# Kernel tuning notes

Hardware: AMD Instinct MI355X
Metric: run time of the kernel (lower is better)

The kernel has to match this reference:

```python
import jax, jax.numpy as jnp
import numpy as np

N, D = 8192, 4096


def setup_inputs() -> dict:
    key = jax.random.key(0)
    k1, k2, k3 = jax.random.split(key, 3)
    x = jax.random.normal(k1, (N, D), jnp.float32)
    W = jax.random.normal(k2, (D, D), jnp.float32) / np.sqrt(D)  # nn.Linear weight [out,in]
    b = jax.random.normal(k3, (D,), jnp.float32) * 0.01
    recency_weight = jnp.full((1,), -0.1, jnp.float32)
    return {"x": x, "W": W, "b": b, "recency_weight": recency_weight}


def reference(x, W, b, recency_weight):
    # linear -> relu projection
    x_proj = jax.nn.relu(x @ W.T + b)  # [N, D]
    # self-similarity
    scores = x_proj @ x_proj.T  # [N, N]
    n = scores.shape[0]
    idx = jnp.arange(n)
    # triu mask with diagonal=0 (use_current_timestep=False): keep strictly lower triangle
    mask = idx[None, :] >= idx[:, None]
    scores = jnp.where(mask, -jnp.inf, scores)
    # recency bias: toeplitz(arange(n)) == |i - j|, zeroed on masked positions
    rec = jnp.abs(idx[:, None] - idx[None, :]).astype(scores.dtype)
    rec = jnp.where(mask, 0.0, rec)
    scores = scores + recency_weight[0] * rec
    # row 0 is fully masked (-inf everywhere); replace with finite values to avoid
    # NaN in softmax -- the row is overwritten with zeros afterwards anyway.
    scores = scores.at[0].set(0.0)
    attn = jax.nn.softmax(scores, axis=1)
    attn = attn.at[0].set(0.0)  # matches scores[0] = zeros in the torch code
    return attn
```

## Files before the change

### kernel.cpp

```cpp
#include <hip/hip_runtime.h>
#include <hip/hip_bf16.h>
#include <stdint.h>

typedef __bf16 bf16_t;
typedef bf16_t bf16x8_t __attribute__((ext_vector_type(8)));
typedef bf16_t bf16x4_t __attribute__((ext_vector_type(4)));
typedef float f32x4_t __attribute__((ext_vector_type(4)));

#define NROWS 8192
#define DDIM  4096
#define BK 32
#define KTILES (DDIM / BK)
#define LSTR 40

__device__ __forceinline__ void gload16(const void* g, void* s) {
  __builtin_amdgcn_global_load_lds(
      (const __attribute__((address_space(1))) void*)g,
      (__attribute__((address_space(3))) void*)s, 16, 0, 0);
}

__global__ __launch_bounds__(256) void k_split(const float* __restrict__ in,
                                               bf16_t* __restrict__ hi,
                                               bf16_t* __restrict__ lo) {
  const long i = ((long)blockIdx.x * 256 + threadIdx.x) * 4;
  const float4 v = *reinterpret_cast<const float4*>(in + i);
  float vv[4] = {v.x, v.y, v.z, v.w};
  bf16x4_t h, l;
#pragma unroll
  for (int c = 0; c < 4; ++c) {
    bf16_t hh = (bf16_t)vv[c];
    h[c] = hh;
    l[c] = (bf16_t)(vv[c] - (float)hh);
  }
  *reinterpret_cast<bf16x4_t*>(hi + i) = h;
  *reinterpret_cast<bf16x4_t*>(lo + i) = l;
}

typedef bf16_t lds_buf_t[4][256][BK];

__device__ __forceinline__ void gemm_core256(
    const bf16_t* __restrict__ pAh, const bf16_t* __restrict__ pAl, long lda,
    const bf16_t* __restrict__ pBh, const bf16_t* __restrict__ pBl, long ldb,
    lds_buf_t* sm, f32x4_t (&acc)[8][4]) {
  const int t = threadIdx.x, lane = t & 63, w = t >> 6;
  const int fr = lane & 15, kg = lane >> 4;
  const int wr = (w >> 2) * 128, wc = (w & 3) * 64;
  const int w32 = w * 32;
  const int sr0 = w32 + (lane >> 2);
  const int sg = (((lane & 3) ^ ((lane >> 3) & 3)) * 8);
  const int kge = (kg ^ ((fr >> 1) & 3)) * 8;

#pragma unroll
  for (int m = 0; m < 8; ++m)
#pragma unroll
    for (int n = 0; n < 4; ++n) acc[m][n] = f32x4_t{0.f, 0.f, 0.f, 0.f};

  const bf16_t* gAh = pAh + (long)sr0 * lda + sg;
  const bf16_t* gAl = pAl + (long)sr0 * lda + sg;
  const bf16_t* gBh = pBh + (long)sr0 * ldb + sg;
  const bf16_t* gBl = pBl + (long)sr0 * ldb + sg;
  const long a16 = 16 * lda, b16 = 16 * ldb;

  auto issue = [&](int buf, int plane, const bf16_t* g, long ld16, int k0) {
    gload16(g + k0, &sm[buf][plane][w32][0]);
    gload16(g + ld16 + k0, &sm[buf][plane][w32 + 16][0]);
  };

  bf16x8_t ah[8], al[8], bh[4], bl[4];
  auto read8 = [&](bf16x8_t(&R)[8], int buf, int plane) {
#pragma unroll
    for (int m = 0; m < 8; ++m)
      R[m] = *reinterpret_cast<const bf16x8_t*>(&sm[buf][plane][wr + m * 16 + fr][kge]);
  };
  auto read4 = [&](bf16x8_t(&R)[4], int buf, int plane) {
#pragma unroll
    for (int n = 0; n < 4; ++n)
      R[n] = *reinterpret_cast<const bf16x8_t*>(&sm[buf][plane][wc + n * 16 + fr][kge]);
  };
  auto mfma32 = [&](bf16x8_t(&A)[8], bf16x8_t(&B)[4]) {
    __builtin_amdgcn_s_setprio(1);
#pragma unroll
    for (int m = 0; m < 8; ++m)
#pragma unroll
      for (int n = 0; n < 4; ++n)
        acc[m][n] = __builtin_amdgcn_mfma_f32_16x16x32_bf16(A[m], B[n], acc[m][n], 0, 0, 0);
    __builtin_amdgcn_s_setprio(0);
  };

  issue(0, 0, gAh, a16, 0);
  issue(0, 2, gBh, b16, 0);
  issue(0, 3, gBl, b16, 0);
  issue(0, 1, gAl, a16, 0);
  asm volatile("s_waitcnt vmcnt(4)" ::: "memory");
  __builtin_amdgcn_s_barrier();

  for (int kt = 0; kt < KTILES - 1; ++kt) {
    const int c = kt & 1;
    const int k0 = (kt + 1) * BK;
    read8(ah, c, 0);
    read4(bh, c, 2);
    issue(c ^ 1, 0, gAh, a16, k0);
    issue(c ^ 1, 2, gBh, b16, k0);
    __builtin_amdgcn_s_barrier();
    mfma32(ah, bh);
    asm volatile("s_waitcnt vmcnt(6)" ::: "memory");
    __builtin_amdgcn_s_barrier();
    read4(bl, c, 3);
    issue(c ^ 1, 3, gBl, b16, k0);
    __builtin_amdgcn_s_barrier();
    mfma32(ah, bl);
    asm volatile("s_waitcnt vmcnt(6)" ::: "memory");
    __builtin_amdgcn_s_barrier();
    read8(al, c, 1);
    issue(c ^ 1, 1, gAl, a16, k0);
    __builtin_amdgcn_s_barrier();
    mfma32(al, bh);
    asm volatile("s_waitcnt vmcnt(4)" ::: "memory");
    __builtin_amdgcn_s_barrier();
  }
  {
    const int c = (KTILES - 1) & 1;
    read8(ah, c, 0);
    read4(bh, c, 2);
    __builtin_amdgcn_s_barrier();
    mfma32(ah, bh);
    asm volatile("s_waitcnt vmcnt(2)" ::: "memory");
    __builtin_amdgcn_s_barrier();
    read4(bl, c, 3);
    __builtin_amdgcn_s_barrier();
    mfma32(ah, bl);
    asm volatile("s_waitcnt vmcnt(0)" ::: "memory");
    __builtin_amdgcn_s_barrier();
    read8(al, c, 1);
    mfma32(al, bh);
  }
}

__global__ __launch_bounds__(512, 2) void k_gemm1_256(
    const bf16_t* __restrict__ xh, const bf16_t* __restrict__ xl,
    const bf16_t* __restrict__ Wh, const bf16_t* __restrict__ Wl,
    const float* __restrict__ bias,
    bf16_t* __restrict__ xph, bf16_t* __restrict__ xpl) {
  extern __shared__ char smraw[];
  lds_buf_t* sm = (lds_buf_t*)smraw;

  int bid = (int)blockIdx.x;
  bid = (bid & 7) * 64 + (bid >> 3);
  const int bx = bid & 15, by = bid >> 4;
  const long brow = (long)by * 256, bcol = (long)bx * 256;

  f32x4_t acc[8][4];
  gemm_core256(xh + brow * DDIM, xl + brow * DDIM, DDIM,
               Wh + bcol * DDIM, Wl + bcol * DDIM, DDIM, sm, acc);

  const int t = threadIdx.x, lane = t & 63, w = t >> 6;
  const int wr = (w >> 2) * 128, wc = (w & 3) * 64;
  const int cr = (lane >> 4) * 4, cc = lane & 15;
#pragma unroll
  for (int n = 0; n < 4; ++n) {
    const long col = bcol + wc + n * 16 + cc;
    const float bb = bias[col];
#pragma unroll
    for (int m = 0; m < 8; ++m) {
      const long row0 = brow + wr + m * 16 + cr;
#pragma unroll
      for (int r = 0; r < 4; ++r) {
        const float v = fmaxf(acc[m][n][r] + bb, 0.f);
        const bf16_t h = (bf16_t)v;
        xph[(row0 + r) * (long)DDIM + col] = h;
        xpl[(row0 + r) * (long)DDIM + col] = (bf16_t)(v - (float)h);
      }
    }
  }
}

__global__ __launch_bounds__(512, 2) void k_gemm2_256(
    const bf16_t* __restrict__ xph, const bf16_t* __restrict__ xpl,
    const float* __restrict__ rwp, float* __restrict__ out) {
  extern __shared__ char smraw[];
  lds_buf_t* sm = (lds_buf_t*)smraw;

  int bid = (int)blockIdx.x;
  bid = (bid & 7) * 66 + (bid >> 3);
  int by = (int)((sqrtf(8.f * (float)bid + 1.f) - 1.f) * 0.5f);
  while ((by + 1) * (by + 2) / 2 <= bid) ++by;
  while (by * (by + 1) / 2 > bid) --by;
  const int bx = bid - by * (by + 1) / 2;

  const long brow = (long)by * 256, bcol = (long)bx * 256;
  f32x4_t acc[8][4];
  gemm_core256(xph + brow * DDIM, xpl + brow * DDIM, DDIM,
               xph + bcol * DDIM, xpl + bcol * DDIM, DDIM, sm, acc);

  const float rw = rwp[0];
  const int t = threadIdx.x, lane = t & 63, w = t >> 6;
  const int wr = (w >> 2) * 128, wc = (w & 3) * 64;
  const int cr = (lane >> 4) * 4, cc = lane & 15;
#pragma unroll
  for (int n = 0; n < 4; ++n) {
    const long gj = bcol + wc + n * 16 + cc;
#pragma unroll
    for (int m = 0; m < 8; ++m) {
      const long gi0 = brow + wr + m * 16 + cr;
#pragma unroll
      for (int r = 0; r < 4; ++r) {
        const long gi = gi0 + r;
        out[gi * (long)NROWS + gj] = acc[m][n][r] + rw * (float)(gi - gj);
      }
    }
  }
}

__device__ __forceinline__ void stage_split(const float* __restrict__ src, long ld,
                                            bf16_t (&hi)[128][LSTR],
                                            bf16_t (&lo)[128][LSTR],
                                            int t) {
#pragma unroll
  for (int i = 0; i < 4; ++i) {
    const int f = i * 256 + t;
    const int row = f >> 3;
    const int kq = (f & 7) << 2;
    const float4 v = *reinterpret_cast<const float4*>(src + (long)row * ld + kq);
    float vv[4] = {v.x, v.y, v.z, v.w};
    bf16x4_t h, l;
#pragma unroll
    for (int c = 0; c < 4; ++c) {
      bf16_t hh = (bf16_t)vv[c];
      h[c] = hh;
      l[c] = (bf16_t)(vv[c] - (float)hh);
    }
    *reinterpret_cast<bf16x4_t*>(&hi[row][kq]) = h;
    *reinterpret_cast<bf16x4_t*>(&lo[row][kq]) = l;
  }
}

__global__ __launch_bounds__(256) void k_gemm1_slow(
    const float* __restrict__ x, const float* __restrict__ W,
    const float* __restrict__ bias,
    bf16_t* __restrict__ xph, bf16_t* __restrict__ xpl) {
  __shared__ alignas(16) bf16_t Ahi[128][LSTR];
  __shared__ alignas(16) bf16_t Alo[128][LSTR];
  __shared__ alignas(16) bf16_t Bhi[128][LSTR];
  __shared__ alignas(16) bf16_t Blo[128][LSTR];

  const long brow = (long)blockIdx.y * 128;
  const long bcol = (long)blockIdx.x * 128;
  const int t = threadIdx.x, lane = t & 63;
  const int wr = ((t >> 6) >> 1) * 64, wc = ((t >> 6) & 1) * 64;
  const int fr = lane & 15, kg = lane >> 4;

  f32x4_t acc[4][4];
#pragma unroll
  for (int m = 0; m < 4; ++m)
#pragma unroll
    for (int n = 0; n < 4; ++n) acc[m][n] = f32x4_t{0.f, 0.f, 0.f, 0.f};

  const float* Abase = x + brow * DDIM;
  const float* Bbase = W + bcol * DDIM;
  for (int k0 = 0; k0 < DDIM; k0 += BK) {
    __syncthreads();
    stage_split(Abase + k0, DDIM, Ahi, Alo, t);
    stage_split(Bbase + k0, DDIM, Bhi, Blo, t);
    __syncthreads();

    bf16x8_t ah[4], al[4], bh[4], bl[4];
#pragma unroll
    for (int m = 0; m < 4; ++m) {
      ah[m] = *reinterpret_cast<const bf16x8_t*>(&Ahi[wr + m * 16 + fr][kg * 8]);
      al[m] = *reinterpret_cast<const bf16x8_t*>(&Alo[wr + m * 16 + fr][kg * 8]);
      bh[m] = *reinterpret_cast<const bf16x8_t*>(&Bhi[wc + m * 16 + fr][kg * 8]);
      bl[m] = *reinterpret_cast<const bf16x8_t*>(&Blo[wc + m * 16 + fr][kg * 8]);
    }
#pragma unroll
    for (int m = 0; m < 4; ++m)
#pragma unroll
      for (int n = 0; n < 4; ++n) {
        acc[m][n] = __builtin_amdgcn_mfma_f32_16x16x32_bf16(ah[m], bh[n], acc[m][n], 0, 0, 0);
        acc[m][n] = __builtin_amdgcn_mfma_f32_16x16x32_bf16(ah[m], bl[n], acc[m][n], 0, 0, 0);
        acc[m][n] = __builtin_amdgcn_mfma_f32_16x16x32_bf16(al[m], bh[n], acc[m][n], 0, 0, 0);
      }
  }

  const int cr = (lane >> 4) * 4, cc = lane & 15;
#pragma unroll
  for (int n = 0; n < 4; ++n) {
    const long col = bcol + wc + n * 16 + cc;
    const float bb = bias[col];
#pragma unroll
    for (int m = 0; m < 4; ++m) {
      const long row0 = brow + wr + m * 16 + cr;
#pragma unroll
      for (int r = 0; r < 4; ++r) {
        const float v = fmaxf(acc[m][n][r] + bb, 0.f);
        const bf16_t h = (bf16_t)v;
        xph[(row0 + r) * (long)DDIM + col] = h;
        xpl[(row0 + r) * (long)DDIM + col] = (bf16_t)(v - (float)h);
      }
    }
  }
}

__global__ __launch_bounds__(256) void k_row_softmax(float* __restrict__ out, int n) {
  const int i = blockIdx.x;
  float* row = out + (size_t)i * n;
  const int L = i;
  const int t = threadIdx.x;
  __shared__ float red[4];

  float m = -3.402823466e+38f;
  for (int j = t; j < L; j += 256) m = fmaxf(m, row[j]);
#pragma unroll
  for (int o = 32; o > 0; o >>= 1) m = fmaxf(m, __shfl_down(m, o, 64));
  if ((t & 63) == 0) red[t >> 6] = m;
  __syncthreads();
  m = fmaxf(fmaxf(red[0], red[1]), fmaxf(red[2], red[3]));
  __syncthreads();

  float s = 0.f;
  for (int j = t; j < L; j += 256) s += expf(row[j] - m);
#pragma unroll
  for (int o = 32; o > 0; o >>= 1) s += __shfl_down(s, o, 64);
  if ((t & 63) == 0) red[t >> 6] = s;
  __syncthreads();
  s = red[0] + red[1] + red[2] + red[3];
  const float inv = (L > 0) ? 1.f / s : 0.f;

  for (int j = t; j < n; j += 256) {
    row[j] = (j < L) ? expf(row[j] - m) * inv : 0.f;
  }
}

extern "C" void kernel_launch(void* const* d_in, const int* in_sizes, int n_in,
                              void* d_out, int out_size, void* d_ws, size_t ws_size,
                              hipStream_t stream) {
  (void)in_sizes; (void)n_in; (void)out_size;
  const float* x = (const float*)d_in[0];
  const float* W = (const float*)d_in[1];
  const float* b = (const float*)d_in[2];
  const float* rw = (const float*)d_in[3];
  float* out = (float*)d_out;

  const size_t NX = (size_t)NROWS * DDIM;
  const size_t NW = (size_t)DDIM * DDIM;
  char* ws = (char*)d_ws;
  bf16_t* xph = (bf16_t*)ws;
  bf16_t* xpl = (bf16_t*)(ws + NX * 2);

  const int LDSB = 2 * 4 * 256 * BK * 2;
  (void)hipFuncSetAttribute(reinterpret_cast<const void*>(k_gemm1_256),
                            hipFuncAttributeMaxDynamicSharedMemorySize, LDSB);
  (void)hipFuncSetAttribute(reinterpret_cast<const void*>(k_gemm2_256),
                            hipFuncAttributeMaxDynamicSharedMemorySize, LDSB);

  const size_t need_full = NX * 4  + NX * 4  + NW * 4 ;
  if (ws_size >= need_full) {
    bf16_t* xh = (bf16_t*)(ws + NX * 4);
    bf16_t* xl = (bf16_t*)(ws + NX * 6);
    bf16_t* Wh = (bf16_t*)(ws + NX * 8);
    bf16_t* Wl = (bf16_t*)(ws + NX * 8 + NW * 2);
    k_split<<<(int)(NX / 1024), 256, 0, stream>>>(x, xh, xl);
    k_split<<<(int)(NW / 1024), 256, 0, stream>>>(W, Wh, Wl);
    k_gemm1_256<<<512, 512, LDSB, stream>>>(xh, xl, Wh, Wl, b, xph, xpl);
  } else {
    k_gemm1_slow<<<dim3(DDIM / 128, NROWS / 128), 256, 0, stream>>>(x, W, b, xph, xpl);
  }

  const int ntri = (NROWS / 256) * (NROWS / 256 + 1) / 2;
  k_gemm2_256<<<ntri, 512, LDSB, stream>>>(xph, xpl, rw, out);
  k_row_softmax<<<NROWS, 256, 0, stream>>>(out, NROWS);
}
```

Before: 1.629 ms.

## Switch split-precision GEMMs to fp16 and drop one cross term in Gram GEMM

All hi/lo splits and MFMA instructions change from bf16 to fp16, which carries more mantissa bits per half. The second GEMM (x_proj @ x_proj^T) now loads only the hi plane for A and computes hi*hi + hi*lo. That drops the lo*hi term, cutting one third of its MFMAs and one plane of LDS traffic, and LDS use shrinks to three planes. The risks are fp16 range overflow for large activations and an asymmetric, less accurate score matrix.

```diff
diff --git a/kernel.cpp b/kernel.cpp
--- a/kernel.cpp
+++ b/kernel.cpp
@@ -2,9 +2,9 @@
 #include <hip/hip_bf16.h>
 #include <stdint.h>
 
-typedef __bf16 bf16_t;
-typedef bf16_t bf16x8_t __attribute__((ext_vector_type(8)));
-typedef bf16_t bf16x4_t __attribute__((ext_vector_type(4)));
+typedef _Float16 f16_t;
+typedef f16_t f16x8_t __attribute__((ext_vector_type(8)));
+typedef f16_t f16x4_t __attribute__((ext_vector_type(4)));
 typedef float f32x4_t __attribute__((ext_vector_type(4)));
 
 #define NROWS 8192
@@ -20,28 +20,28 @@
 }
 
 __global__ __launch_bounds__(256) void k_split(const float* __restrict__ in,
-                                               bf16_t* __restrict__ hi,
-                                               bf16_t* __restrict__ lo) {
+                                               f16_t* __restrict__ hi,
+                                               f16_t* __restrict__ lo) {
   const long i = ((long)blockIdx.x * 256 + threadIdx.x) * 4;
   const float4 v = *reinterpret_cast<const float4*>(in + i);
   float vv[4] = {v.x, v.y, v.z, v.w};
-  bf16x4_t h, l;
+  f16x4_t h, l;
 #pragma unroll
   for (int c = 0; c < 4; ++c) {
-    bf16_t hh = (bf16_t)vv[c];
+    f16_t hh = (f16_t)vv[c];
     h[c] = hh;
-    l[c] = (bf16_t)(vv[c] - (float)hh);
-  }
-  *reinterpret_cast<bf16x4_t*>(hi + i) = h;
-  *reinterpret_cast<bf16x4_t*>(lo + i) = l;
-}
-
-typedef bf16_t lds_buf_t[4][256][BK];
-
-__device__ __forceinline__ void gemm_core256(
-    const bf16_t* __restrict__ pAh, const bf16_t* __restrict__ pAl, long lda,
-    const bf16_t* __restrict__ pBh, const bf16_t* __restrict__ pBl, long ldb,
-    lds_buf_t* sm, f32x4_t (&acc)[8][4]) {
+    l[c] = (f16_t)(vv[c] - (float)hh);
+  }
+  *reinterpret_cast<f16x4_t*>(hi + i) = h;
+  *reinterpret_cast<f16x4_t*>(lo + i) = l;
+}
+
+typedef f16_t lds4_t[4][256][BK];
+
+__device__ __forceinline__ void gemm_core256_3p(
+    const f16_t* __restrict__ pAh, const f16_t* __restrict__ pAl, long lda,
+    const f16_t* __restrict__ pBh, const f16_t* __restrict__ pBl, long ldb,
+    lds4_t* sm, f32x4_t (&acc)[8][4]) {
   const int t = threadIdx.x, lane = t & 63, w = t >> 6;
   const int fr = lane & 15, kg = lane >> 4;
   const int wr = (w >> 2) * 128, wc = (w & 3) * 64;
@@ -55,35 +55,35 @@
 #pragma unroll
     for (int n = 0; n < 4; ++n) acc[m][n] = f32x4_t{0.f, 0.f, 0.f, 0.f};
 
-  const bf16_t* gAh = pAh + (long)sr0 * lda + sg;
-  const bf16_t* gAl = pAl + (long)sr0 * lda + sg;
-  const bf16_t* gBh = pBh + (long)sr0 * ldb + sg;
-  const bf16_t* gBl = pBl + (long)sr0 * ldb + sg;
+  const f16_t* gAh = pAh + (long)sr0 * lda + sg;
+  const f16_t* gAl = pAl + (long)sr0 * lda + sg;
+  const f16_t* gBh = pBh + (long)sr0 * ldb + sg;
+  const f16_t* gBl = pBl + (long)sr0 * ldb + sg;
   const long a16 = 16 * lda, b16 = 16 * ldb;
 
-  auto issue = [&](int buf, int plane, const bf16_t* g, long ld16, int k0) {
+  auto issue = [&](int buf, int plane, const f16_t* g, long ld16, int k0) {
     gload16(g + k0, &sm[buf][plane][w32][0]);
     gload16(g + ld16 + k0, &sm[buf][plane][w32 + 16][0]);
   };
 
-  bf16x8_t ah[8], al[8], bh[4], bl[4];
-  auto read8 = [&](bf16x8_t(&R)[8], int buf, int plane) {
+  f16x8_t ah[8], al[8], bh[4], bl[4];
+  auto read8 = [&](f16x8_t(&R)[8], int buf, int plane) {
 #pragma unroll
     for (int m = 0; m < 8; ++m)
-      R[m] = *reinterpret_cast<const bf16x8_t*>(&sm[buf][plane][wr + m * 16 + fr][kge]);
-  };
-  auto read4 = [&](bf16x8_t(&R)[4], int buf, int plane) {
+      R[m] = *reinterpret_cast<const f16x8_t*>(&sm[buf][plane][wr + m * 16 + fr][kge]);
+  };
+  auto read4 = [&](f16x8_t(&R)[4], int buf, int plane) {
 #pragma unroll
     for (int n = 0; n < 4; ++n)
-      R[n] = *reinterpret_cast<const bf16x8_t*>(&sm[buf][plane][wc + n * 16 + fr][kge]);
-  };
-  auto mfma32 = [&](bf16x8_t(&A)[8], bf16x8_t(&B)[4]) {
+      R[n] = *reinterpret_cast<const f16x8_t*>(&sm[buf][plane][wc + n * 16 + fr][kge]);
+  };
+  auto mfma32 = [&](f16x8_t(&A)[8], f16x8_t(&B)[4]) {
     __builtin_amdgcn_s_setprio(1);
 #pragma unroll
     for (int m = 0; m < 8; ++m)
 #pragma unroll
       for (int n = 0; n < 4; ++n)
-        acc[m][n] = __builtin_amdgcn_mfma_f32_16x16x32_bf16(A[m], B[n], acc[m][n], 0, 0, 0);
+        acc[m][n] = __builtin_amdgcn_mfma_f32_16x16x32_f16(A[m], B[n], acc[m][n], 0, 0, 0);
     __builtin_amdgcn_s_setprio(0);
   };
 
@@ -136,13 +136,100 @@
   }
 }
 
+typedef f16_t lds3_t[3][256][BK];
+
+__device__ __forceinline__ void gemm_core256_2p(
+    const f16_t* __restrict__ pAh, long lda,
+    const f16_t* __restrict__ pBh, const f16_t* __restrict__ pBl, long ldb,
+    lds3_t* sm, f32x4_t (&acc)[8][4]) {
+  const int t = threadIdx.x, lane = t & 63, w = t >> 6;
+  const int fr = lane & 15, kg = lane >> 4;
+  const int wr = (w >> 2) * 128, wc = (w & 3) * 64;
+  const int w32 = w * 32;
+  const int sr0 = w32 + (lane >> 2);
+  const int sg = (((lane & 3) ^ ((lane >> 3) & 3)) * 8);
+  const int kge = (kg ^ ((fr >> 1) & 3)) * 8;
+
+#pragma unroll
+  for (int m = 0; m < 8; ++m)
+#pragma unroll
+    for (int n = 0; n < 4; ++n) acc[m][n] = f32x4_t{0.f, 0.f, 0.f, 0.f};
+
+  const f16_t* gAh = pAh + (long)sr0 * lda + sg;
+  const f16_t* gBh = pBh + (long)sr0 * ldb + sg;
+  const f16_t* gBl = pBl + (long)sr0 * ldb + sg;
+  const long a16 = 16 * lda, b16 = 16 * ldb;
+
+  auto issue = [&](int buf, int plane, const f16_t* g, long ld16, int k0) {
+    gload16(g + k0, &sm[buf][plane][w32][0]);
+    gload16(g + ld16 + k0, &sm[buf][plane][w32 + 16][0]);
+  };
+
+  f16x8_t ah[8], bh[4], bl[4];
+  auto read8 = [&](f16x8_t(&R)[8], int buf, int plane) {
+#pragma unroll
+    for (int m = 0; m < 8; ++m)
+      R[m] = *reinterpret_cast<const f16x8_t*>(&sm[buf][plane][wr + m * 16 + fr][kge]);
+  };
+  auto read4 = [&](f16x8_t(&R)[4], int buf, int plane) {
+#pragma unroll
+    for (int n = 0; n < 4; ++n)
+      R[n] = *reinterpret_cast<const f16x8_t*>(&sm[buf][plane][wc + n * 16 + fr][kge]);
+  };
+  auto mfma32 = [&](f16x8_t(&A)[8], f16x8_t(&B)[4]) {
+    __builtin_amdgcn_s_setprio(1);
+#pragma unroll
+    for (int m = 0; m < 8; ++m)
+#pragma unroll
+      for (int n = 0; n < 4; ++n)
+        acc[m][n] = __builtin_amdgcn_mfma_f32_16x16x32_f16(A[m], B[n], acc[m][n], 0, 0, 0);
+    __builtin_amdgcn_s_setprio(0);
+  };
+
+  issue(0, 0, gAh, a16, 0);
+  issue(0, 1, gBh, b16, 0);
+  issue(0, 2, gBl, b16, 0);
+  asm volatile("s_waitcnt vmcnt(2)" ::: "memory");
+  __builtin_amdgcn_s_barrier();
+
+  for (int kt = 0; kt < KTILES - 1; ++kt) {
+    const int c = kt & 1;
+    const int k0 = (kt + 1) * BK;
+    read8(ah, c, 0);
+    read4(bh, c, 1);
+    issue(c ^ 1, 0, gAh, a16, k0);
+    issue(c ^ 1, 1, gBh, b16, k0);
+    __builtin_amdgcn_s_barrier();
+    mfma32(ah, bh);
+    asm volatile("s_waitcnt vmcnt(4)" ::: "memory");
+    __builtin_amdgcn_s_barrier();
+    read4(bl, c, 2);
+    issue(c ^ 1, 2, gBl, b16, k0);
+    __builtin_amdgcn_s_barrier();
+    mfma32(ah, bl);
+    asm volatile("s_waitcnt vmcnt(2)" ::: "memory");
+    __builtin_amdgcn_s_barrier();
+  }
+  {
+    const int c = (KTILES - 1) & 1;
+    read8(ah, c, 0);
+    read4(bh, c, 1);
+    __builtin_amdgcn_s_barrier();
+    mfma32(ah, bh);
+    asm volatile("s_waitcnt vmcnt(0)" ::: "memory");
+    __builtin_amdgcn_s_barrier();
+    read4(bl, c, 2);
+    mfma32(ah, bl);
+  }
+}
+
 __global__ __launch_bounds__(512, 2) void k_gemm1_256(
-    const bf16_t* __restrict__ xh, const bf16_t* __restrict__ xl,
-    const bf16_t* __restrict__ Wh, const bf16_t* __restrict__ Wl,
+    const f16_t* __restrict__ xh, const f16_t* __restrict__ xl,
+    const f16_t* __restrict__ Wh, const f16_t* __restrict__ Wl,
     const float* __restrict__ bias,
-    bf16_t* __restrict__ xph, bf16_t* __restrict__ xpl) {
+    f16_t* __restrict__ xph, f16_t* __restrict__ xpl) {
   extern __shared__ char smraw[];
-  lds_buf_t* sm = (lds_buf_t*)smraw;
+  lds4_t* sm = (lds4_t*)smraw;
 
   int bid = (int)blockIdx.x;
   bid = (bid & 7) * 64 + (bid >> 3);
@@ -150,8 +237,8 @@
   const long brow = (long)by * 256, bcol = (long)bx * 256;
 
   f32x4_t acc[8][4];
-  gemm_core256(xh + brow * DDIM, xl + brow * DDIM, DDIM,
-               Wh + bcol * DDIM, Wl + bcol * DDIM, DDIM, sm, acc);
+  gemm_core256_3p(xh + brow * DDIM, xl + brow * DDIM, DDIM,
+                  Wh + bcol * DDIM, Wl + bcol * DDIM, DDIM, sm, acc);
 
   const int t = threadIdx.x, lane = t & 63, w = t >> 6;
   const int wr = (w >> 2) * 128, wc = (w & 3) * 64;
@@ -166,19 +253,19 @@
 #pragma unroll
       for (int r = 0; r < 4; ++r) {
         const float v = fmaxf(acc[m][n][r] + bb, 0.f);
-        const bf16_t h = (bf16_t)v;
+        const f16_t h = (f16_t)v;
         xph[(row0 + r) * (long)DDIM + col] = h;
-        xpl[(row0 + r) * (long)DDIM + col] = (bf16_t)(v - (float)h);
+        xpl[(row0 + r) * (long)DDIM + col] = (f16_t)(v - (float)h);
       }
     }
   }
 }
 
 __global__ __launch_bounds__(512, 2) void k_gemm2_256(
-    const bf16_t* __restrict__ xph, const bf16_t* __restrict__ xpl,
+    const f16_t* __restrict__ xph, const f16_t* __restrict__ xpl,
     const float* __restrict__ rwp, float* __restrict__ out) {
   extern __shared__ char smraw[];
-  lds_buf_t* sm = (lds_buf_t*)smraw;
+  lds3_t* sm = (lds3_t*)smraw;
 
   int bid = (int)blockIdx.x;
   bid = (bid & 7) * 66 + (bid >> 3);
@@ -189,8 +276,8 @@
 
   const long brow = (long)by * 256, bcol = (long)bx * 256;
   f32x4_t acc[8][4];
-  gemm_core256(xph + brow * DDIM, xpl + brow * DDIM, DDIM,
-               xph + bcol * DDIM, xpl + bcol * DDIM, DDIM, sm, acc);
+  gemm_core256_2p(xph + brow * DDIM, DDIM,
+                  xph + bcol * DDIM, xpl + bcol * DDIM, DDIM, sm, acc);
 
   const float rw = rwp[0];
   const int t = threadIdx.x, lane = t & 63, w = t >> 6;
@@ -212,8 +299,8 @@
 }
 
 __device__ __forceinline__ void stage_split(const float* __restrict__ src, long ld,
-                                            bf16_t (&hi)[128][LSTR],
-                                            bf16_t (&lo)[128][LSTR],
+                                            f16_t (&hi)[128][LSTR],
+                                            f16_t (&lo)[128][LSTR],
                                             int t) {
 #pragma unroll
   for (int i = 0; i < 4; ++i) {
@@ -222,26 +309,26 @@
     const int kq = (f & 7) << 2;
     const float4 v = *reinterpret_cast<const float4*>(src + (long)row * ld + kq);
     float vv[4] = {v.x, v.y, v.z, v.w};
-    bf16x4_t h, l;
+    f16x4_t h, l;
 #pragma unroll
     for (int c = 0; c < 4; ++c) {
-      bf16_t hh = (bf16_t)vv[c];
+      f16_t hh = (f16_t)vv[c];
       h[c] = hh;
-      l[c] = (bf16_t)(vv[c] - (float)hh);
+      l[c] = (f16_t)(vv[c] - (float)hh);
     }
-    *reinterpret_cast<bf16x4_t*>(&hi[row][kq]) = h;
-    *reinterpret_cast<bf16x4_t*>(&lo[row][kq]) = l;
+    *reinterpret_cast<f16x4_t*>(&hi[row][kq]) = h;
+    *reinterpret_cast<f16x4_t*>(&lo[row][kq]) = l;
   }
 }
 
 __global__ __launch_bounds__(256) void k_gemm1_slow(
     const float* __restrict__ x, const float* __restrict__ W,
     const float* __restrict__ bias,
-    bf16_t* __restrict__ xph, bf16_t* __restrict__ xpl) {
-  __shared__ alignas(16) bf16_t Ahi[128][LSTR];
-  __shared__ alignas(16) bf16_t Alo[128][LSTR];
-  __shared__ alignas(16) bf16_t Bhi[128][LSTR];
-  __shared__ alignas(16) bf16_t Blo[128][LSTR];
+    f16_t* __restrict__ xph, f16_t* __restrict__ xpl) {
+  __shared__ alignas(16) f16_t Ahi[128][LSTR];
+  __shared__ alignas(16) f16_t Alo[128][LSTR];
+  __shared__ alignas(16) f16_t Bhi[128][LSTR];
+  __shared__ alignas(16) f16_t Blo[128][LSTR];
 
   const long brow = (long)blockIdx.y * 128;
   const long bcol = (long)blockIdx.x * 128;
@@ -263,21 +350,21 @@
     stage_split(Bbase + k0, DDIM, Bhi, Blo, t);
     __syncthreads();
 
-    bf16x8_t ah[4], al[4], bh[4], bl[4];
+    f16x8_t ah[4], al[4], bh[4], bl[4];
 #pragma unroll
     for (int m = 0; m < 4; ++m) {
-      ah[m] = *reinterpret_cast<const bf16x8_t*>(&Ahi[wr + m * 16 + fr][kg * 8]);
-      al[m] = *reinterpret_cast<const bf16x8_t*>(&Alo[wr + m * 16 + fr][kg * 8]);
-      bh[m] = *reinterpret_cast<const bf16x8_t*>(&Bhi[wc + m * 16 + fr][kg * 8]);
-      bl[m] = *reinterpret_cast<const bf16x8_t*>(&Blo[wc + m * 16 + fr][kg * 8]);
+      ah[m] = *reinterpret_cast<const f16x8_t*>(&Ahi[wr + m * 16 + fr][kg * 8]);
+      al[m] = *reinterpret_cast<const f16x8_t*>(&Alo[wr + m * 16 + fr][kg * 8]);
+      bh[m] = *reinterpret_cast<const f16x8_t*>(&Bhi[wc + m * 16 + fr][kg * 8]);
+      bl[m] = *reinterpret_cast<const f16x8_t*>(&Blo[wc + m * 16 + fr][kg * 8]);
     }
 #pragma unroll
     for (int m = 0; m < 4; ++m)
 #pragma unroll
       for (int n = 0; n < 4; ++n) {
-        acc[m][n] = __builtin_amdgcn_mfma_f32_16x16x32_bf16(ah[m], bh[n], acc[m][n], 0, 0, 0);
-        acc[m][n] = __builtin_amdgcn_mfma_f32_16x16x32_bf16(ah[m], bl[n], acc[m][n], 0, 0, 0);
-        acc[m][n] = __builtin_amdgcn_mfma_f32_16x16x32_bf16(al[m], bh[n], acc[m][n], 0, 0, 0);
+        acc[m][n] = __builtin_amdgcn_mfma_f32_16x16x32_f16(ah[m], bh[n], acc[m][n], 0, 0, 0);
+        acc[m][n] = __builtin_amdgcn_mfma_f32_16x16x32_f16(ah[m], bl[n], acc[m][n], 0, 0, 0);
+        acc[m][n] = __builtin_amdgcn_mfma_f32_16x16x32_f16(al[m], bh[n], acc[m][n], 0, 0, 0);
       }
   }
 
@@ -292,9 +379,9 @@
 #pragma unroll
       for (int r = 0; r < 4; ++r) {
         const float v = fmaxf(acc[m][n][r] + bb, 0.f);
-        const bf16_t h = (bf16_t)v;
+        const f16_t h = (f16_t)v;
         xph[(row0 + r) * (long)DDIM + col] = h;
-        xpl[(row0 + r) * (long)DDIM + col] = (bf16_t)(v - (float)h);
+        xpl[(row0 + r) * (long)DDIM + col] = (f16_t)(v - (float)h);
       }
     }
   }
@@ -343,29 +430,30 @@
   const size_t NX = (size_t)NROWS * DDIM;
   const size_t NW = (size_t)DDIM * DDIM;
   char* ws = (char*)d_ws;
-  bf16_t* xph = (bf16_t*)ws;
-  bf16_t* xpl = (bf16_t*)(ws + NX * 2);
-
-  const int LDSB = 2 * 4 * 256 * BK * 2;
+  f16_t* xph = (f16_t*)ws;
+  f16_t* xpl = (f16_t*)(ws + NX * 2);
+
+  const int LDSB1 = 2 * 4 * 256 * BK * 2;
+  const int LDSB2 = 2 * 3 * 256 * BK * 2;
   (void)hipFuncSetAttribute(reinterpret_cast<const void*>(k_gemm1_256),
-                            hipFuncAttributeMaxDynamicSharedMemorySize, LDSB);
+                            hipFuncAttributeMaxDynamicSharedMemorySize, LDSB1);
   (void)hipFuncSetAttribute(reinterpret_cast<const void*>(k_gemm2_256),
-                            hipFuncAttributeMaxDynamicSharedMemorySize, LDSB);
+                            hipFuncAttributeMaxDynamicSharedMemorySize, LDSB2);
 
   const size_t need_full = NX * 4  + NX * 4  + NW * 4 ;
   if (ws_size >= need_full) {
-    bf16_t* xh = (bf16_t*)(ws + NX * 4);
-    bf16_t* xl = (bf16_t*)(ws + NX * 6);
-    bf16_t* Wh = (bf16_t*)(ws + NX * 8);
-    bf16_t* Wl = (bf16_t*)(ws + NX * 8 + NW * 2);
+    f16_t* xh = (f16_t*)(ws + NX * 4);
+    f16_t* xl = (f16_t*)(ws + NX * 6);
+    f16_t* Wh = (f16_t*)(ws + NX * 8);
+    f16_t* Wl = (f16_t*)(ws + NX * 8 + NW * 2);
     k_split<<<(int)(NX / 1024), 256, 0, stream>>>(x, xh, xl);
     k_split<<<(int)(NW / 1024), 256, 0, stream>>>(W, Wh, Wl);
-    k_gemm1_256<<<512, 512, LDSB, stream>>>(xh, xl, Wh, Wl, b, xph, xpl);
+    k_gemm1_256<<<512, 512, LDSB1, stream>>>(xh, xl, Wh, Wl, b, xph, xpl);
   } else {
     k_gemm1_slow<<<dim3(DDIM / 128, NROWS / 128), 256, 0, stream>>>(x, W, b, xph, xpl);
   }
 
   const int ntri = (NROWS / 256) * (NROWS / 256 + 1) / 2;
-  k_gemm2_256<<<ntri, 512, LDSB, stream>>>(xph, xpl, rw, out);
+  k_gemm2_256<<<ntri, 512, LDSB2, stream>>>(xph, xpl, rw, out);
   k_row_softmax<<<NROWS, 256, 0, stream>>>(out, NROWS);
 }
```

After: 1.408 ms. 1.16x faster.
